# Performance work log

Hardware: AMD Instinct MI355X
Metric: run time of the kernel (lower is better)

The kernel has to match this reference:

```python
import jax, jax.numpy as jnp
import numpy as np

D = 1024          # d_model
E = 12            # n_routed
HS = 2 * D        # shared hidden (r_shared=2)
HR = 3 * D        # routed hidden (r_routed=3)
TAU = 1.5         # router temperature


def setup_inputs() -> dict:
    key = jax.random.key(0)
    ks = jax.random.split(key, 12)
    def xavier(k, shape):
        fan_in, fan_out = shape[-2], shape[-1]
        lim = jnp.sqrt(6.0 / (fan_in + fan_out))
        return jax.random.uniform(k, shape, jnp.float32, -lim, lim)
    x = jax.random.normal(ks[0], (2, 1024, D), jnp.float32)
    # shared expert (n_shared=1, GEGLU)
    Ws1 = xavier(ks[1], (D, 2 * HS)); bs1 = jnp.zeros((2 * HS,), jnp.float32)
    Ws2 = xavier(ks[2], (HS, D));     bs2 = jnp.zeros((D,), jnp.float32)
    # routed experts, stacked [E, ...]
    We1 = xavier(ks[3], (E, D, 2 * HR)); be1 = jnp.zeros((E, 2 * HR), jnp.float32)
    We2 = xavier(ks[4], (E, HR, D));     be2 = jnp.zeros((E, D), jnp.float32)
    # router
    Wr = xavier(ks[5], (D, E)); br = jnp.zeros((E,), jnp.float32)
    return {"x": x, "Ws1": Ws1, "bs1": bs1, "Ws2": Ws2, "bs2": bs2,
            "We1": We1, "be1": be1, "We2": We2, "be2": be2, "Wr": Wr, "br": br}


def _geglu(h):
    a, g = jnp.split(h, 2, axis=-1)
    return a * jax.nn.gelu(g, approximate=False)  # torch GELU is exact erf


def reference(x, Ws1, bs1, Ws2, bs2, We1, be1, We2, be2, Wr, br):
    B, T, Dm = x.shape
    xf = x.reshape(-1, Dm)                                   # [N, D]
    # shared expert (n_shared=1 -> divide by 1)
    ys = _geglu(xf @ Ws1 + bs1) @ Ws2 + bs2                  # [N, D]
    # top-2 router (eval: no noise)
    logits = (xf @ Wr + br) / TAU                            # [N, E]
    top_val, top_idx = jax.lax.top_k(logits, 2)              # [N, 2]
    top_w = jax.nn.softmax(top_val, axis=-1)                 # [N, 2]
    # combine weights per (token, expert); non-selected experts get 0
    onehot = jax.nn.one_hot(top_idx, E, dtype=x.dtype)       # [N, 2, E]
    w = jnp.einsum('nke,nk->ne', onehot, top_w)              # [N, E]
    # dropless dense dispatch: every expert sees all tokens, weight 0 masks
    h = jnp.einsum('nd,edh->enh', xf, We1) + be1[:, None, :] # [E, N, 2*HR]
    act = _geglu(h)                                          # [E, N, HR]
    yE = jnp.einsum('enh,ehd->end', act, We2) + be2[:, None, :]
    yr = jnp.einsum('end,ne->nd', yE, w)                     # [N, D]
    return (ys + yr).reshape(B, T, Dm)
```

## Files before the change

### kernel.cpp

```cpp
#include <hip/hip_runtime.h>

#define N_TOK 2048
#define DMODEL 1024
#define NEXP 12
#define HS_DIM 2048
#define HR_DIM 3072

typedef __attribute__((ext_vector_type(8))) short bf16x8;
typedef __attribute__((ext_vector_type(16))) float f32x16;

#define AS1 __attribute__((address_space(1)))
#define AS3 __attribute__((address_space(3)))

__device__ __forceinline__ void gl_lds16(const void* g, void* l) {
  __builtin_amdgcn_global_load_lds((const AS1 void*)g, (AS3 void*)l, 16, 0, 0);
}

__device__ __forceinline__ unsigned short f2bf(float x) {
  union { float f; unsigned int u; } v; v.f = x;
  unsigned int u = v.u;
  u += 0x7fff + ((u >> 16) & 1);
  return (unsigned short)(u >> 16);
}
__device__ __forceinline__ unsigned pack2(float a, float b) {
  return (unsigned)f2bf(a) | ((unsigned)f2bf(b) << 16);
}
__device__ __forceinline__ float gelu_exact(float x) {
  return 0.5f * x * (1.0f + erff(x * 0.70710678118654752f));
}


__global__ __launch_bounds__(256)
void convert_x_kernel(const float* __restrict__ X, unsigned short* __restrict__ XB) {
  const int idx = (blockIdx.x * 256 + threadIdx.x) * 8;
  float4 f0 = *(const float4*)(X + idx);
  float4 f1 = *(const float4*)(X + idx + 4);
  uint4 o;
  o.x = pack2(f0.x, f0.y); o.y = pack2(f0.z, f0.w);
  o.z = pack2(f1.x, f1.y); o.w = pack2(f1.z, f1.w);
  *(uint4*)(XB + idx) = o;
}

__global__ __launch_bounds__(256)
void tconv_kernel(const float* __restrict__ W, unsigned short* __restrict__ WT,
                  int K, int N) {
  const int n0 = blockIdx.x * 64;
  const int k0 = blockIdx.y * 64;
  const size_t bo = (size_t)blockIdx.z * K * N;
  __shared__ __align__(16) unsigned short Ts[64 * 72];
  const int t = threadIdx.x;
  const int k4 = (t >> 4) * 4, n4 = (t & 15) * 4;
  float4 rw[4];
#pragma unroll
  for (int i = 0; i < 4; ++i)
    rw[i] = *(const float4*)(W + bo + (size_t)(k0 + k4 + i) * N + n0 + n4);
#pragma unroll
  for (int j = 0; j < 4; ++j) {
    uint2 v;
    v.x = pack2(((const float*)&rw[0])[j], ((const float*)&rw[1])[j]);
    v.y = pack2(((const float*)&rw[2])[j], ((const float*)&rw[3])[j]);
    *(uint2*)&Ts[(n4 + j) * 72 + k4] = v;
  }
  __syncthreads();
  const int n = t >> 2, kc = (t & 3) * 16;
  uint4 v0 = *(const uint4*)&Ts[n * 72 + kc];
  uint4 v1 = *(const uint4*)&Ts[n * 72 + kc + 8];
  unsigned short* dst = WT + (size_t)blockIdx.z * N * K + (size_t)(n0 + n) * K + k0 + kc;
  *(uint4*)dst = v0;
  *(uint4*)(dst + 8) = v1;
}


__global__ void init_kernel(int* counts, int* cursors) {
  int t = threadIdx.x;
  if (t < NEXP) { counts[t] = 0; cursors[t] = 0; }
}

__global__ __launch_bounds__(256)
void router_kernel(const float* __restrict__ X, const float* __restrict__ Wr,
                   const float* __restrict__ br, int* __restrict__ top_e,
                   float* __restrict__ top_w, int* __restrict__ counts) {
  const int wv = threadIdx.x >> 6, lane = threadIdx.x & 63;
  const int n = blockIdx.x * 4 + wv;
  float a[NEXP];
#pragma unroll
  for (int e = 0; e < NEXP; ++e) a[e] = 0.f;
  for (int it = 0; it < DMODEL / 64; ++it) {
    int k = it * 64 + lane;
    float xv = X[(size_t)n * DMODEL + k];
    const float* wr = Wr + (size_t)k * NEXP;
#pragma unroll
    for (int e = 0; e < NEXP; ++e) a[e] += xv * wr[e];
  }
#pragma unroll
  for (int e = 0; e < NEXP; ++e)
    for (int o = 32; o > 0; o >>= 1) a[e] += __shfl_xor(a[e], o, 64);
  if (lane == 0) {
    float l[NEXP];
#pragma unroll
    for (int e = 0; e < NEXP; ++e) l[e] = (a[e] + br[e]) * (1.0f / 1.5f);
    int e0 = 0;
    for (int e = 1; e < NEXP; ++e) if (l[e] > l[e0]) e0 = e;
    int e1 = (e0 == 0) ? 1 : 0;
    for (int e = 0; e < NEXP; ++e) if (e != e0 && l[e] > l[e1]) e1 = e;
    float w0 = 1.f / (1.f + expf(l[e1] - l[e0]));
    top_e[n * 2 + 0] = e0; top_e[n * 2 + 1] = e1;
    top_w[n * 2 + 0] = w0; top_w[n * 2 + 1] = 1.f - w0;
    atomicAdd(&counts[e0], 1); atomicAdd(&counts[e1], 1);
  }
}

__global__ void scan_kernel(const int* __restrict__ counts, int* __restrict__ offs) {
  if (threadIdx.x == 0) {
    int s = 0;
    for (int e = 0; e < NEXP; ++e) { offs[e] = s; s += counts[e]; }
    offs[NEXP] = s;
  }
}

__global__ __launch_bounds__(256)
void fill_kernel(const int* __restrict__ top_e, const float* __restrict__ top_w,
                 const int* __restrict__ offs, int* __restrict__ cursors,
                 int* __restrict__ slot_tok, float* __restrict__ slot_w) {
  int n = blockIdx.x * 256 + threadIdx.x;
  if (n >= N_TOK) return;
#pragma unroll
  for (int j = 0; j < 2; ++j) {
    int e = top_e[n * 2 + j];
    int p = atomicAdd(&cursors[e], 1);
    int s = offs[e] + p;
    slot_tok[s] = n;
    slot_w[s] = top_w[n * 2 + j];
  }
}

__global__ __launch_bounds__(256)
void zero_out_kernel(float4* __restrict__ out) {
  out[blockIdx.x * 256 + threadIdx.x] = make_float4(0.f, 0.f, 0.f, 0.f);
}

#define G1_SHARED 256
#define G1_PER_E  384

__global__ __launch_bounds__(256, 2)
void gemm1_all_kernel(const unsigned short* __restrict__ XB,
                      const unsigned short* __restrict__ WS,
                      const unsigned short* __restrict__ WE,
                      const float* __restrict__ BSb, const float* __restrict__ BEb,
                      unsigned short* __restrict__ ACT_S, unsigned short* __restrict__ ACT_R,
                      const int* __restrict__ slot_tok, const int* __restrict__ offs,
                      const int* __restrict__ counts) {
  int id = blockIdx.x;
  const unsigned short* W; const float* bias; unsigned short* ACT;
  int H, count, off, m0, n0, routed;
  if (id < G1_SHARED) {
    routed = 0;
    m0 = (id >> 4) * 128; n0 = (id & 15) * 128;
    W = WS; bias = BSb; ACT = ACT_S; H = HS_DIM; count = N_TOK; off = 0;
  } else {
    routed = 1;
    id -= G1_SHARED;
    const int e = id / G1_PER_E, rem = id % G1_PER_E;
    m0 = (rem / 24) * 128; n0 = (rem % 24) * 128;
    W = WE + (size_t)e * 2 * HR_DIM * DMODEL;
    bias = BEb + (size_t)e * 2 * HR_DIM;
    ACT = ACT_R; H = HR_DIM; count = counts[e]; off = offs[e];
  }
  if (m0 >= count) return;

  __shared__ __align__(16) unsigned short As[2 * 4096];
  __shared__ __align__(16) unsigned short Bs[2 * 8192];

  const int t = threadIdx.x;
  const int lane = t & 63, wv = t >> 6;
  const int srow = t >> 2, skc = t & 3;
  const int ln31 = lane & 31, hi = lane >> 5;
  const int wr = wv >> 1, wc = wv & 1;

  const unsigned short* ap[2];
#pragma unroll
  for (int g = 0; g < 2; ++g) {
    int mr = m0 + srow + 64 * g;
    int tok;
    if (routed) {
      int s = off + (mr < count ? mr : count - 1);
      tok = slot_tok[s];
    } else {
      tok = mr;
    }
    ap[g] = XB + (size_t)tok * DMODEL + skc * 8;
  }
  const unsigned short* bp[4];
#pragma unroll
  for (int g = 0; g < 4; ++g) {
    int brow = srow + 64 * g;
    int wrow = (brow < 128) ? (n0 + brow) : (H + n0 + brow - 128);
    bp[g] = W + (size_t)wrow * DMODEL + skc * 8;
  }

  f32x16 acc_a[2][2], acc_g[2][2];
  const f32x16 z16 = {0.f,0.f,0.f,0.f,0.f,0.f,0.f,0.f,0.f,0.f,0.f,0.f,0.f,0.f,0.f,0.f};
#pragma unroll
  for (int i = 0; i < 2; ++i)
#pragma unroll
    for (int j = 0; j < 2; ++j) { acc_a[i][j] = z16; acc_g[i][j] = z16; }

  for (int kt = 0; kt < DMODEL / 64; ++kt) {
    const int kb = kt * 64;
    __syncthreads();
#pragma unroll
    for (int h = 0; h < 2; ++h) {
#pragma unroll
      for (int g = 0; g < 2; ++g)
        gl_lds16(ap[g] + kb + h * 32, &As[h * 4096 + g * 2048 + wv * 512]);
#pragma unroll
      for (int g = 0; g < 4; ++g)
        gl_lds16(bp[g] + kb + h * 32, &Bs[h * 8192 + g * 2048 + wv * 512]);
    }
    __syncthreads();
#pragma unroll
    for (int ks = 0; ks < 4; ++ks) {
      const int h = ks >> 1;
      const int ko = (ks & 1) * 16 + hi * 8;
      bf16x8 aF[2], bA[2], bG[2];
#pragma unroll
      for (int i = 0; i < 2; ++i)
        aF[i] = *(const bf16x8*)&As[h * 4096 + (wr * 64 + i * 32 + ln31) * 32 + ko];
#pragma unroll
      for (int j = 0; j < 2; ++j) {
        bA[j] = *(const bf16x8*)&Bs[h * 8192 + (wc * 64 + j * 32 + ln31) * 32 + ko];
        bG[j] = *(const bf16x8*)&Bs[h * 8192 + (128 + wc * 64 + j * 32 + ln31) * 32 + ko];
      }
#pragma unroll
      for (int i = 0; i < 2; ++i)
#pragma unroll
        for (int j = 0; j < 2; ++j) {
          acc_a[i][j] = __builtin_amdgcn_mfma_f32_32x32x16_bf16(aF[i], bA[j], acc_a[i][j], 0, 0, 0);
          acc_g[i][j] = __builtin_amdgcn_mfma_f32_32x32x16_bf16(aF[i], bG[j], acc_g[i][j], 0, 0, 0);
        }
    }
  }

  float ba[2], bg[2];
#pragma unroll
  for (int j = 0; j < 2; ++j) {
    int col = n0 + wc * 64 + j * 32 + ln31;
    ba[j] = bias[col];
    bg[j] = bias[H + col];
  }
#pragma unroll
  for (int i = 0; i < 2; ++i)
#pragma unroll
    for (int j = 0; j < 2; ++j)
#pragma unroll
      for (int reg = 0; reg < 16; ++reg) {
        int row = wr * 64 + i * 32 + (reg & 3) + 8 * (reg >> 2) + 4 * hi;
        if (m0 + row < count) {
          int col = n0 + wc * 64 + j * 32 + ln31;
          float av = acc_a[i][j][reg] + ba[j];
          float gv = acc_g[i][j][reg] + bg[j];
          ACT[(size_t)(off + m0 + row) * H + col] = f2bf(av * gelu_exact(gv));
        }
      }
}

#define G2_SHARED 256
#define G2_PER_E  384
#define G2_KCHUNK 1024

__global__ __launch_bounds__(256, 2)
void gemm2_all_kernel(const unsigned short* __restrict__ ACT_S,
                      const unsigned short* __restrict__ ACT_R,
                      const unsigned short* __restrict__ WSt,
                      const unsigned short* __restrict__ WEt,
                      const float* __restrict__ BSb, const float* __restrict__ BEb,
                      float* __restrict__ OUT,
                      const int* __restrict__ slot_tok, const float* __restrict__ slot_w,
                      const int* __restrict__ offs, const int* __restrict__ counts) {
  int id = blockIdx.x;
  const unsigned short* A; const unsigned short* W; const float* bias;
  int K, count, off, m0, n0, routed, kc;
  if (id < G2_SHARED) {
    routed = 0;
    kc = id & 1;
    const int rem2 = id >> 1;
    m0 = (rem2 >> 3) * 128; n0 = (rem2 & 7) * 128;
    A = ACT_S; W = WSt; bias = BSb; K = HS_DIM; count = N_TOK; off = 0;
  } else {
    routed = 1;
    id -= G2_SHARED;
    const int e = id / G2_PER_E, rem = id % G2_PER_E;
    kc = rem % 3;
    const int rem2 = rem / 3;
    m0 = (rem2 >> 3) * 128; n0 = (rem2 & 7) * 128;
    A = ACT_R; W = WEt + (size_t)e * DMODEL * HR_DIM;
    bias = BEb + (size_t)e * DMODEL; K = HR_DIM; count = counts[e]; off = offs[e];
  }
  if (m0 >= count) return;

  __shared__ __align__(16) unsigned short As[2 * 4096];
  __shared__ __align__(16) unsigned short Bs[2 * 4096];

  const int t = threadIdx.x;
  const int lane = t & 63, wv = t >> 6;
  const int srow = t >> 2, skc = t & 3;
  const int ln31 = lane & 31, hi = lane >> 5;
  const int wr = wv >> 1, wc = wv & 1;

  const unsigned short* ap[2];
#pragma unroll
  for (int g = 0; g < 2; ++g) {
    int mr = m0 + srow + 64 * g;
    int r = off + (mr < count ? mr : count - 1);
    ap[g] = A + (size_t)r * K + skc * 8;
  }
  const unsigned short* bp[2];
#pragma unroll
  for (int g = 0; g < 2; ++g)
    bp[g] = W + (size_t)(n0 + srow + 64 * g) * K + skc * 8;

  f32x16 acc[2][2];
  const f32x16 z16 = {0.f,0.f,0.f,0.f,0.f,0.f,0.f,0.f,0.f,0.f,0.f,0.f,0.f,0.f,0.f,0.f};
#pragma unroll
  for (int i = 0; i < 2; ++i)
#pragma unroll
    for (int j = 0; j < 2; ++j) acc[i][j] = z16;

  const int kt0 = kc * (G2_KCHUNK >> 6);
  const int kt1 = kt0 + (G2_KCHUNK >> 6);
  for (int kt = kt0; kt < kt1; ++kt) {
    const int kb = kt * 64;
    __syncthreads();
#pragma unroll
    for (int h = 0; h < 2; ++h) {
#pragma unroll
      for (int g = 0; g < 2; ++g) {
        gl_lds16(ap[g] + kb + h * 32, &As[h * 4096 + g * 2048 + wv * 512]);
        gl_lds16(bp[g] + kb + h * 32, &Bs[h * 4096 + g * 2048 + wv * 512]);
      }
    }
    __syncthreads();
#pragma unroll
    for (int ks = 0; ks < 4; ++ks) {
      const int h = ks >> 1;
      const int ko = (ks & 1) * 16 + hi * 8;
      bf16x8 aF[2], bF[2];
#pragma unroll
      for (int i = 0; i < 2; ++i)
        aF[i] = *(const bf16x8*)&As[h * 4096 + (wr * 64 + i * 32 + ln31) * 32 + ko];
#pragma unroll
      for (int j = 0; j < 2; ++j)
        bF[j] = *(const bf16x8*)&Bs[h * 4096 + (wc * 64 + j * 32 + ln31) * 32 + ko];
#pragma unroll
      for (int i = 0; i < 2; ++i)
#pragma unroll
        for (int j = 0; j < 2; ++j)
          acc[i][j] = __builtin_amdgcn_mfma_f32_32x32x16_bf16(aF[i], bF[j], acc[i][j], 0, 0, 0);
    }
  }

  float bb[2];
#pragma unroll
  for (int j = 0; j < 2; ++j)
    bb[j] = (kc == 0) ? bias[n0 + wc * 64 + j * 32 + ln31] : 0.f;
#pragma unroll
  for (int i = 0; i < 2; ++i)
#pragma unroll
    for (int j = 0; j < 2; ++j)
#pragma unroll
      for (int reg = 0; reg < 16; ++reg) {
        int row = wr * 64 + i * 32 + (reg & 3) + 8 * (reg >> 2) + 4 * hi;
        if (m0 + row < count) {
          int col = n0 + wc * 64 + j * 32 + ln31;
          float v = acc[i][j][reg] + bb[j];
          if (routed) {
            int s = off + m0 + row;
            atomicAdd(&OUT[(size_t)slot_tok[s] * DMODEL + col], slot_w[s] * v);
          } else {
            atomicAdd(&OUT[(size_t)(m0 + row) * DMODEL + col], v);
          }
        }
      }
}


extern "C" void kernel_launch(void* const* d_in, const int* in_sizes, int n_in,
                              void* d_out, int out_size, void* d_ws, size_t ws_size,
                              hipStream_t stream) {
  const float* x   = (const float*)d_in[0];
  const float* Ws1 = (const float*)d_in[1];
  const float* bs1 = (const float*)d_in[2];
  const float* Ws2 = (const float*)d_in[3];
  const float* bs2 = (const float*)d_in[4];
  const float* We1 = (const float*)d_in[5];
  const float* be1 = (const float*)d_in[6];
  const float* We2 = (const float*)d_in[7];
  const float* be2 = (const float*)d_in[8];
  const float* Wr  = (const float*)d_in[9];
  const float* br  = (const float*)d_in[10];
  float* out = (float*)d_out;

  char* p = (char*)d_ws;
  int* counts  = (int*)p; p += 256;
  int* cursors = (int*)p; p += 256;
  int* offs    = (int*)p; p += 256;
  int* top_e   = (int*)p; p += (size_t)N_TOK * 2 * 4;
  float* top_w = (float*)p; p += (size_t)N_TOK * 2 * 4;
  int* slot_tok = (int*)p; p += (size_t)2 * N_TOK * 4;
  float* slot_w = (float*)p; p += (size_t)2 * N_TOK * 4;
  unsigned short* xb    = (unsigned short*)p; p += (size_t)N_TOK * DMODEL * 2;
  unsigned short* ws1t  = (unsigned short*)p; p += (size_t)2 * HS_DIM * DMODEL * 2;
  unsigned short* ws2t  = (unsigned short*)p; p += (size_t)DMODEL * HS_DIM * 2;
  unsigned short* we1t  = (unsigned short*)p; p += (size_t)NEXP * 2 * HR_DIM * DMODEL * 2;
  unsigned short* we2t  = (unsigned short*)p; p += (size_t)NEXP * DMODEL * HR_DIM * 2;
  unsigned short* act_s = (unsigned short*)p; p += (size_t)N_TOK * HS_DIM * 2;
  unsigned short* act_r = (unsigned short*)p; p += (size_t)2 * N_TOK * HR_DIM * 2;

  zero_out_kernel<<<(N_TOK * DMODEL) / 1024, 256, 0, stream>>>((float4*)out);

  convert_x_kernel<<<(N_TOK * DMODEL) / 2048, 256, 0, stream>>>(x, xb);
  tconv_kernel<<<dim3(2 * HS_DIM / 64, DMODEL / 64, 1), 256, 0, stream>>>(Ws1, ws1t, DMODEL, 2 * HS_DIM);
  tconv_kernel<<<dim3(DMODEL / 64, HS_DIM / 64, 1), 256, 0, stream>>>(Ws2, ws2t, HS_DIM, DMODEL);
  tconv_kernel<<<dim3(2 * HR_DIM / 64, DMODEL / 64, NEXP), 256, 0, stream>>>(We1, we1t, DMODEL, 2 * HR_DIM);
  tconv_kernel<<<dim3(DMODEL / 64, HR_DIM / 64, NEXP), 256, 0, stream>>>(We2, we2t, HR_DIM, DMODEL);

  init_kernel<<<1, 64, 0, stream>>>(counts, cursors);
  router_kernel<<<N_TOK / 4, 256, 0, stream>>>(x, Wr, br, top_e, top_w, counts);
  scan_kernel<<<1, 64, 0, stream>>>(counts, offs);
  fill_kernel<<<N_TOK / 256, 256, 0, stream>>>(top_e, top_w, offs, cursors, slot_tok, slot_w);

  gemm1_all_kernel<<<G1_SHARED + G1_PER_E * NEXP, 256, 0, stream>>>(
      xb, ws1t, we1t, bs1, be1, act_s, act_r, slot_tok, offs, counts);

  gemm2_all_kernel<<<G2_SHARED + G2_PER_E * NEXP, 256, 0, stream>>>(
      act_s, act_r, ws2t, we2t, bs2, be2, out, slot_tok, slot_w, offs, counts);
}
```

Baseline: 940.0 us.

## Double-buffer GEMM K loop, swizzle LDS, replace atomics with partial-sum combine

```diff
diff --git a/kernel.cpp b/kernel.cpp
--- a/kernel.cpp
+++ b/kernel.cpp
@@ -5,6 +5,7 @@
 #define NEXP 12
 #define HS_DIM 2048
 #define HR_DIM 3072
+#define NSLOT (2 * N_TOK)
 
 typedef __attribute__((ext_vector_type(8))) short bf16x8;
 typedef __attribute__((ext_vector_type(16))) float f32x16;
@@ -121,7 +122,8 @@
 __global__ __launch_bounds__(256)
 void fill_kernel(const int* __restrict__ top_e, const float* __restrict__ top_w,
                  const int* __restrict__ offs, int* __restrict__ cursors,
-                 int* __restrict__ slot_tok, float* __restrict__ slot_w) {
+                 int* __restrict__ slot_tok, float* __restrict__ slot_w,
+                 int* __restrict__ tok_slot) {
   int n = blockIdx.x * 256 + threadIdx.x;
   if (n >= N_TOK) return;
 #pragma unroll
@@ -131,12 +133,8 @@
     int s = offs[e] + p;
     slot_tok[s] = n;
     slot_w[s] = top_w[n * 2 + j];
-  }
-}
-
-__global__ __launch_bounds__(256)
-void zero_out_kernel(float4* __restrict__ out) {
-  out[blockIdx.x * 256 + threadIdx.x] = make_float4(0.f, 0.f, 0.f, 0.f);
+    tok_slot[n * 2 + j] = s;
+  }
 }
 
 #define G1_SHARED 256
@@ -176,6 +174,7 @@
   const int srow = t >> 2, skc = t & 3;
   const int ln31 = lane & 31, hi = lane >> 5;
   const int wr = wv >> 1, wc = wv & 1;
+  const int skc_s = skc ^ ((srow >> 1) & 3);
 
   const unsigned short* ap[2];
 #pragma unroll
@@ -188,14 +187,14 @@
     } else {
       tok = mr;
     }
-    ap[g] = XB + (size_t)tok * DMODEL + skc * 8;
+    ap[g] = XB + (size_t)tok * DMODEL + skc_s * 8;
   }
   const unsigned short* bp[4];
 #pragma unroll
   for (int g = 0; g < 4; ++g) {
     int brow = srow + 64 * g;
     int wrow = (brow < 128) ? (n0 + brow) : (H + n0 + brow - 128);
-    bp[g] = W + (size_t)wrow * DMODEL + skc * 8;
+    bp[g] = W + (size_t)wrow * DMODEL + skc_s * 8;
   }
 
   f32x16 acc_a[2][2], acc_g[2][2];
@@ -205,31 +204,36 @@
 #pragma unroll
     for (int j = 0; j < 2; ++j) { acc_a[i][j] = z16; acc_g[i][j] = z16; }
 
-  for (int kt = 0; kt < DMODEL / 64; ++kt) {
-    const int kb = kt * 64;
-    __syncthreads();
-#pragma unroll
-    for (int h = 0; h < 2; ++h) {
-#pragma unroll
-      for (int g = 0; g < 2; ++g)
-        gl_lds16(ap[g] + kb + h * 32, &As[h * 4096 + g * 2048 + wv * 512]);
-#pragma unroll
-      for (int g = 0; g < 4; ++g)
-        gl_lds16(bp[g] + kb + h * 32, &Bs[h * 8192 + g * 2048 + wv * 512]);
-    }
-    __syncthreads();
-#pragma unroll
-    for (int ks = 0; ks < 4; ++ks) {
-      const int h = ks >> 1;
-      const int ko = (ks & 1) * 16 + hi * 8;
+#define G1_STAGE(B, KB)                                                   \
+  {                                                                       \
+    _Pragma("unroll") for (int g = 0; g < 2; ++g)                         \
+        gl_lds16(ap[g] + (KB), &As[(B) * 4096 + g * 2048 + wv * 512]);    \
+    _Pragma("unroll") for (int g = 0; g < 4; ++g)                         \
+        gl_lds16(bp[g] + (KB), &Bs[(B) * 8192 + g * 2048 + wv * 512]);    \
+  }
+
+  int buf = 0;
+  G1_STAGE(0, 0)
+  for (int kt = 0; kt < DMODEL / 32; ++kt) {
+    asm volatile("s_waitcnt vmcnt(0)" ::: "memory");
+    __builtin_amdgcn_s_barrier();
+    if (kt + 1 < DMODEL / 32) { G1_STAGE(buf ^ 1, (kt + 1) * 32) }
+#pragma unroll
+    for (int ks = 0; ks < 2; ++ks) {
+      const int ko = ks * 16 + hi * 8;
+      const int ch = ko >> 3;
       bf16x8 aF[2], bA[2], bG[2];
 #pragma unroll
-      for (int i = 0; i < 2; ++i)
-        aF[i] = *(const bf16x8*)&As[h * 4096 + (wr * 64 + i * 32 + ln31) * 32 + ko];
+      for (int i = 0; i < 2; ++i) {
+        int r = wr * 64 + i * 32 + ln31;
+        aF[i] = *(const bf16x8*)&As[buf * 4096 + r * 32 + ((ch ^ ((r >> 1) & 3)) << 3)];
+      }
 #pragma unroll
       for (int j = 0; j < 2; ++j) {
-        bA[j] = *(const bf16x8*)&Bs[h * 8192 + (wc * 64 + j * 32 + ln31) * 32 + ko];
-        bG[j] = *(const bf16x8*)&Bs[h * 8192 + (128 + wc * 64 + j * 32 + ln31) * 32 + ko];
+        int r = wc * 64 + j * 32 + ln31;
+        bA[j] = *(const bf16x8*)&Bs[buf * 8192 + r * 32 + ((ch ^ ((r >> 1) & 3)) << 3)];
+        int r2 = 128 + r;
+        bG[j] = *(const bf16x8*)&Bs[buf * 8192 + r2 * 32 + ((ch ^ ((r2 >> 1) & 3)) << 3)];
       }
 #pragma unroll
       for (int i = 0; i < 2; ++i)
@@ -239,7 +243,9 @@
           acc_g[i][j] = __builtin_amdgcn_mfma_f32_32x32x16_bf16(aF[i], bG[j], acc_g[i][j], 0, 0, 0);
         }
     }
-  }
+    buf ^= 1;
+  }
+#undef G1_STAGE
 
   float ba[2], bg[2];
 #pragma unroll
@@ -266,16 +272,14 @@
 
 #define G2_SHARED 256
 #define G2_PER_E  384
-#define G2_KCHUNK 1024
-
-__global__ __launch_bounds__(256, 2)
+
+__global__ __launch_bounds__(256, 4)
 void gemm2_all_kernel(const unsigned short* __restrict__ ACT_S,
                       const unsigned short* __restrict__ ACT_R,
                       const unsigned short* __restrict__ WSt,
                       const unsigned short* __restrict__ WEt,
                       const float* __restrict__ BSb, const float* __restrict__ BEb,
-                      float* __restrict__ OUT,
-                      const int* __restrict__ slot_tok, const float* __restrict__ slot_w,
+                      float* __restrict__ SP, float* __restrict__ YP,
                       const int* __restrict__ offs, const int* __restrict__ counts) {
   int id = blockIdx.x;
   const unsigned short* A; const unsigned short* W; const float* bias;
@@ -306,18 +310,19 @@
   const int srow = t >> 2, skc = t & 3;
   const int ln31 = lane & 31, hi = lane >> 5;
   const int wr = wv >> 1, wc = wv & 1;
+  const int skc_s = skc ^ ((srow >> 1) & 3);
 
   const unsigned short* ap[2];
 #pragma unroll
   for (int g = 0; g < 2; ++g) {
     int mr = m0 + srow + 64 * g;
     int r = off + (mr < count ? mr : count - 1);
-    ap[g] = A + (size_t)r * K + skc * 8;
+    ap[g] = A + (size_t)r * K + skc_s * 8;
   }
   const unsigned short* bp[2];
 #pragma unroll
   for (int g = 0; g < 2; ++g)
-    bp[g] = W + (size_t)(n0 + srow + 64 * g) * K + skc * 8;
+    bp[g] = W + (size_t)(n0 + srow + 64 * g) * K + skc_s * 8;
 
   f32x16 acc[2][2];
   const f32x16 z16 = {0.f,0.f,0.f,0.f,0.f,0.f,0.f,0.f,0.f,0.f,0.f,0.f,0.f,0.f,0.f,0.f};
@@ -326,38 +331,45 @@
 #pragma unroll
     for (int j = 0; j < 2; ++j) acc[i][j] = z16;
 
-  const int kt0 = kc * (G2_KCHUNK >> 6);
-  const int kt1 = kt0 + (G2_KCHUNK >> 6);
-  for (int kt = kt0; kt < kt1; ++kt) {
-    const int kb = kt * 64;
-    __syncthreads();
-#pragma unroll
-    for (int h = 0; h < 2; ++h) {
-#pragma unroll
-      for (int g = 0; g < 2; ++g) {
-        gl_lds16(ap[g] + kb + h * 32, &As[h * 4096 + g * 2048 + wv * 512]);
-        gl_lds16(bp[g] + kb + h * 32, &Bs[h * 4096 + g * 2048 + wv * 512]);
-      }
-    }
-    __syncthreads();
-#pragma unroll
-    for (int ks = 0; ks < 4; ++ks) {
-      const int h = ks >> 1;
-      const int ko = (ks & 1) * 16 + hi * 8;
+#define G2_STAGE(B, KB)                                                   \
+  {                                                                       \
+    _Pragma("unroll") for (int g = 0; g < 2; ++g) {                       \
+      gl_lds16(ap[g] + (KB), &As[(B) * 4096 + g * 2048 + wv * 512]);      \
+      gl_lds16(bp[g] + (KB), &Bs[(B) * 4096 + g * 2048 + wv * 512]);      \
+    }                                                                     \
+  }
+
+  const int kb0 = kc * 1024;
+  int buf = 0;
+  G2_STAGE(0, kb0)
+  for (int kt = 0; kt < 32; ++kt) {
+    asm volatile("s_waitcnt vmcnt(0)" ::: "memory");
+    __builtin_amdgcn_s_barrier();
+    if (kt + 1 < 32) { G2_STAGE(buf ^ 1, kb0 + (kt + 1) * 32) }
+#pragma unroll
+    for (int ks = 0; ks < 2; ++ks) {
+      const int ko = ks * 16 + hi * 8;
+      const int ch = ko >> 3;
       bf16x8 aF[2], bF[2];
 #pragma unroll
-      for (int i = 0; i < 2; ++i)
-        aF[i] = *(const bf16x8*)&As[h * 4096 + (wr * 64 + i * 32 + ln31) * 32 + ko];
-#pragma unroll
-      for (int j = 0; j < 2; ++j)
-        bF[j] = *(const bf16x8*)&Bs[h * 4096 + (wc * 64 + j * 32 + ln31) * 32 + ko];
+      for (int i = 0; i < 2; ++i) {
+        int r = wr * 64 + i * 32 + ln31;
+        aF[i] = *(const bf16x8*)&As[buf * 4096 + r * 32 + ((ch ^ ((r >> 1) & 3)) << 3)];
+      }
+#pragma unroll
+      for (int j = 0; j < 2; ++j) {
+        int r = wc * 64 + j * 32 + ln31;
+        bF[j] = *(const bf16x8*)&Bs[buf * 4096 + r * 32 + ((ch ^ ((r >> 1) & 3)) << 3)];
+      }
 #pragma unroll
       for (int i = 0; i < 2; ++i)
 #pragma unroll
         for (int j = 0; j < 2; ++j)
           acc[i][j] = __builtin_amdgcn_mfma_f32_32x32x16_bf16(aF[i], bF[j], acc[i][j], 0, 0, 0);
     }
-  }
+    buf ^= 1;
+  }
+#undef G2_STAGE
 
   float bb[2];
 #pragma unroll
@@ -374,13 +386,35 @@
           int col = n0 + wc * 64 + j * 32 + ln31;
           float v = acc[i][j][reg] + bb[j];
           if (routed) {
-            int s = off + m0 + row;
-            atomicAdd(&OUT[(size_t)slot_tok[s] * DMODEL + col], slot_w[s] * v);
+            YP[((size_t)kc * NSLOT + off + m0 + row) * DMODEL + col] = v;
           } else {
-            atomicAdd(&OUT[(size_t)(m0 + row) * DMODEL + col], v);
+            SP[((size_t)kc * N_TOK + m0 + row) * DMODEL + col] = v;
           }
         }
       }
+}
+
+__global__ __launch_bounds__(256)
+void combine_kernel(const float* __restrict__ SP, const float* __restrict__ YP,
+                    const int* __restrict__ tok_slot, const float* __restrict__ slot_w,
+                    float* __restrict__ OUT) {
+  const int n = blockIdx.x;
+  const int tx = threadIdx.x;
+  const int s0 = tok_slot[n * 2 + 0], s1 = tok_slot[n * 2 + 1];
+  const float w0 = slot_w[s0], w1 = slot_w[s1];
+  float4 r = ((const float4*)(SP + (size_t)n * DMODEL))[tx];
+  float4 b = ((const float4*)(SP + (size_t)(N_TOK + n) * DMODEL))[tx];
+  r.x += b.x; r.y += b.y; r.z += b.z; r.w += b.w;
+#pragma unroll
+  for (int kc = 0; kc < 3; ++kc) {
+    float4 p0 = ((const float4*)(YP + ((size_t)kc * NSLOT + s0) * DMODEL))[tx];
+    float4 p1 = ((const float4*)(YP + ((size_t)kc * NSLOT + s1) * DMODEL))[tx];
+    r.x += w0 * p0.x + w1 * p1.x;
+    r.y += w0 * p0.y + w1 * p1.y;
+    r.z += w0 * p0.z + w1 * p1.z;
+    r.w += w0 * p0.w + w1 * p1.w;
+  }
+  ((float4*)(OUT + (size_t)n * DMODEL))[tx] = r;
 }
 
 
@@ -406,17 +440,18 @@
   int* offs    = (int*)p; p += 256;
   int* top_e   = (int*)p; p += (size_t)N_TOK * 2 * 4;
   float* top_w = (float*)p; p += (size_t)N_TOK * 2 * 4;
-  int* slot_tok = (int*)p; p += (size_t)2 * N_TOK * 4;
-  float* slot_w = (float*)p; p += (size_t)2 * N_TOK * 4;
+  int* slot_tok = (int*)p; p += (size_t)NSLOT * 4;
+  float* slot_w = (float*)p; p += (size_t)NSLOT * 4;
+  int* tok_slot = (int*)p; p += (size_t)N_TOK * 2 * 4;
   unsigned short* xb    = (unsigned short*)p; p += (size_t)N_TOK * DMODEL * 2;
   unsigned short* ws1t  = (unsigned short*)p; p += (size_t)2 * HS_DIM * DMODEL * 2;
   unsigned short* ws2t  = (unsigned short*)p; p += (size_t)DMODEL * HS_DIM * 2;
   unsigned short* we1t  = (unsigned short*)p; p += (size_t)NEXP * 2 * HR_DIM * DMODEL * 2;
   unsigned short* we2t  = (unsigned short*)p; p += (size_t)NEXP * DMODEL * HR_DIM * 2;
   unsigned short* act_s = (unsigned short*)p; p += (size_t)N_TOK * HS_DIM * 2;
-  unsigned short* act_r = (unsigned short*)p; p += (size_t)2 * N_TOK * HR_DIM * 2;
-
-  zero_out_kernel<<<(N_TOK * DMODEL) / 1024, 256, 0, stream>>>((float4*)out);
+  unsigned short* act_r = (unsigned short*)p; p += (size_t)NSLOT * HR_DIM * 2;
+  float* sp = (float*)p; p += (size_t)2 * N_TOK * DMODEL * 4;
+  float* yp = (float*)p; p += (size_t)3 * NSLOT * DMODEL * 4;
 
   convert_x_kernel<<<(N_TOK * DMODEL) / 2048, 256, 0, stream>>>(x, xb);
   tconv_kernel<<<dim3(2 * HS_DIM / 64, DMODEL / 64, 1), 256, 0, stream>>>(Ws1, ws1t, DMODEL, 2 * HS_DIM);
@@ -427,11 +462,13 @@
   init_kernel<<<1, 64, 0, stream>>>(counts, cursors);
   router_kernel<<<N_TOK / 4, 256, 0, stream>>>(x, Wr, br, top_e, top_w, counts);
   scan_kernel<<<1, 64, 0, stream>>>(counts, offs);
-  fill_kernel<<<N_TOK / 256, 256, 0, stream>>>(top_e, top_w, offs, cursors, slot_tok, slot_w);
+  fill_kernel<<<N_TOK / 256, 256, 0, stream>>>(top_e, top_w, offs, cursors, slot_tok, slot_w, tok_slot);
 
   gemm1_all_kernel<<<G1_SHARED + G1_PER_E * NEXP, 256, 0, stream>>>(
       xb, ws1t, we1t, bs1, be1, act_s, act_r, slot_tok, offs, counts);
 
   gemm2_all_kernel<<<G2_SHARED + G2_PER_E * NEXP, 256, 0, stream>>>(
-      act_s, act_r, ws2t, we2t, bs2, be2, out, slot_tok, slot_w, offs, counts);
-}
+      act_s, act_r, ws2t, we2t, bs2, be2, sp, yp, offs, counts);
+
+  combine_kernel<<<N_TOK, 256, 0, stream>>>(sp, yp, tok_slot, slot_w, out);
+}
```

Result: faster. 890.4 us (-5.3%).
